# Kernel tuning notes

Hardware: AMD Instinct MI355X
Metric: run time of the kernel (lower is better)

The kernel has to match this reference:

```python
import jax, jax.numpy as jnp
import numpy as np

T, B, E, H = 2048, 2, 2048, 16
D = E // H  # 128


def setup_inputs() -> dict:
    key = jax.random.key(0)
    ks = jax.random.split(key, 4)
    query = jax.random.normal(ks[0], (T, B, E), dtype=jnp.float32)
    Wqkv = jax.random.normal(ks[1], (3 * E, E), dtype=jnp.float32) * 0.02
    bqkv = jnp.zeros((3 * E,), dtype=jnp.float32)
    Wo = jax.random.normal(ks[2], (E, E), dtype=jnp.float32) * 0.02
    bo = jnp.zeros((E,), dtype=jnp.float32)
    # Llama rotary frequencies: freqs_cis[t, j] = exp(i * t * theta^{-2j/D})
    inv_freq = 1.0 / (10000.0 ** (np.arange(0, D, 2, dtype=np.float32) / D))  # (D/2,)
    angles = np.arange(T, dtype=np.float32)[:, None] * inv_freq[None, :]       # (T, D/2)
    freqs_cos = jnp.asarray(np.cos(angles), dtype=jnp.float32)
    freqs_sin = jnp.asarray(np.sin(angles), dtype=jnp.float32)
    return {"query": query, "Wqkv": Wqkv, "bqkv": bqkv, "Wo": Wo, "bo": bo,
            "freqs_cos": freqs_cos, "freqs_sin": freqs_sin}


def _apply_rope(x, cos, sin):
    # Faithful to metaseq: x is (T, B, E) but view()-ed as (B, T, H, D);
    # jnp.reshape is the same row-major reinterpretation as torch .view().
    xr = x.reshape(B, T, H, D // 2, 2)
    x0, x1 = xr[..., 0], xr[..., 1]
    c = cos[None, :, None, :]  # broadcast over batch and heads, seq_dim=1
    s = sin[None, :, None, :]
    o0 = x0 * c - x1 * s
    o1 = x0 * s + x1 * c
    return jnp.stack([o0, o1], axis=-1).reshape(T, B, E)


def reference(query, Wqkv, bqkv, Wo, bo, freqs_cos, freqs_sin):
    # Combined QKV projection (ColumnParallelLinear, world_size=1), split order (k, v, q)
    kvq = jnp.einsum('tbe,fe->tbf', query, Wqkv) + bqkv  # (T, B, 3E)
    k, v, q = jnp.split(kvq, 3, axis=-1)
    q = _apply_rope(q, freqs_cos, freqs_sin)
    k = _apply_rope(k, freqs_cos, freqs_sin)
    # scaling split as sqrt(head_dim^-0.5) on both q and k (baddbmm path)
    s = jnp.asarray(D, jnp.float32) ** -0.25
    qb = q.reshape(T, B * H, D).swapaxes(0, 1) * s   # (BH, T, D)
    kb = k.reshape(T, B * H, D).swapaxes(0, 1) * s   # (BH, S, D)
    vb = v.reshape(T, B * H, D).swapaxes(0, 1)       # (BH, S, D)
    scores = jnp.einsum('btd,bsd->bts', qb, kb)      # (BH, T, S)
    causal = jnp.tril(jnp.ones((T, T), dtype=bool))  # ScaledUpperTriangMaskedSoftmax
    scores = jnp.where(causal[None, :, :], scores, jnp.finfo(scores.dtype).min)
    probs = jax.nn.softmax(scores, axis=-1)          # dropout p=0 -> identity
    attn = jnp.einsum('bts,bsd->btd', probs, vb)     # (BH, T, D)
    attn = attn.swapaxes(0, 1).reshape(T, B, E)
    # RowParallelLinear with skip_bias_add=True: bias returned separately (not added)
    out = jnp.einsum('tbe,fe->tbf', attn, Wo)
    return out
```

## Files before the change

### kernel.cpp

```cpp
#include <hip/hip_runtime.h>
#include <stdint.h>

typedef unsigned short u16;
typedef __attribute__((ext_vector_type(4))) float f32x4;
typedef __attribute__((ext_vector_type(8))) short bf16x8;
typedef __attribute__((ext_vector_type(8))) u16 u16x8;

#define T_SEQ  2048
#define EMB    2048
#define HD     128
#define NHEAD  16
#define NE3    6144
#define SCALE  0.29730177875068026f
#define LOG2E  1.44269504088896f

typedef __attribute__((address_space(3))) char* lds_t;
typedef const __attribute__((address_space(1))) char* gl_t;

__device__ __forceinline__ void gld16(const void* g, void* l) {
  __builtin_amdgcn_global_load_lds((gl_t)g, (lds_t)l, 16, 0, 0);
}

__device__ __forceinline__ u16 f2bf(float f) {
  union { float f; uint32_t u; } c; c.f = f;
  uint32_t r = c.u + 0x7fffu + ((c.u >> 16) & 1u);
  return (u16)(r >> 16);
}

__global__ __launch_bounds__(256) void cvt_bf16(const float* __restrict__ in,
                                                u16* __restrict__ out, int n8) {
  int i = blockIdx.x * 256 + threadIdx.x;
  if (i >= n8) return;
  const float4* p = (const float4*)in + (size_t)i * 2;
  float4 a = p[0], b = p[1];
  u16x8 o;
  o[0]=f2bf(a.x); o[1]=f2bf(a.y); o[2]=f2bf(a.z); o[3]=f2bf(a.w);
  o[4]=f2bf(b.x); o[5]=f2bf(b.y); o[6]=f2bf(b.z); o[7]=f2bf(b.w);
  *((u16x8*)out + i) = o;
}

__device__ __forceinline__ bf16x8 rdfrag(const char* slot, int row, int lq) {
  return *(const bf16x8*)(slot + row*64 + ((lq ^ ((row >> 1) & 3)) << 4));
}
__device__ __forceinline__ void stg512(const char* g, int K2, int kbyte,
                                       char* slot, int j, int tid) {
  int lb = j*8192 + tid*16;
  int row = lb >> 6, c = (lb >> 4) & 3;
  gld16(g + (size_t)row*K2 + kbyte + ((c ^ ((row >> 1) & 3)) << 4), slot + lb);
}

template<int EPI>
__global__ __launch_bounds__(512, 2) void gemmF(
    const u16* __restrict__ A, const u16* __restrict__ Bm, int K, int N,
    const float* __restrict__ cosT, const float* __restrict__ sinT,
    const float* __restrict__ bias,
    u16* __restrict__ Qh, u16* __restrict__ Kh, u16* __restrict__ Vt,
    float* __restrict__ Cout)
{
  __shared__ __align__(16) char lds[98304];
  const int tid = threadIdx.x;
  const int lane = tid & 63, w = tid >> 6;
  const int wm = w >> 2, wn = w & 3;
  const int l15 = lane & 15, lq = lane >> 4;

  const int i = blockIdx.x;
  const int r = i >> 8, x = i & 7, s = (i >> 3) & 31;
  const int regionId = r*8 + x;
  const int bM = (regionId & 3)*8 + (s >> 2);
  const int bN = (regionId >> 2)*4 + (s & 3);

  const char* Ag = (const char*)(A + (size_t)bM * 128 * K);
  const char* Bg = (const char*)(Bm + (size_t)bN * 256 * K);
  const int K2 = K * 2;
  const int nT = K >> 5;

  #define BUF(k) (lds + ((k) & 3) * 24576)
  #define STAGE(t) do { int kb_ = (t) << 6; char* b_ = BUF(t);        \
    stg512(Ag, K2, kb_, b_, 0, tid);                                  \
    stg512(Bg, K2, kb_, b_ + 8192, 0, tid);                           \
    stg512(Bg, K2, kb_, b_ + 8192, 1, tid); } while (0)

  STAGE(0); STAGE(1); STAGE(2);
  asm volatile("s_waitcnt vmcnt(6)" ::: "memory");
  __builtin_amdgcn_s_barrier();
  __builtin_amdgcn_sched_barrier(0);

  bf16x8 afA[4], bfA[4], afB[4], bfB[4];
  #pragma unroll
  for (int j = 0; j < 4; j++) afA[j] = rdfrag(BUF(0), wm*64 + j*16 + l15, lq);
  #pragma unroll
  for (int j = 0; j < 4; j++) bfA[j] = rdfrag(BUF(0) + 8192, wn*64 + j*16 + l15, lq);

  f32x4 acc[4][4] = {};

  #define ITER(t, CA, CB, OA, OB) do {                                     \
    asm volatile("s_waitcnt vmcnt(3)" ::: "memory");  \
    __builtin_amdgcn_s_barrier();                                          \
    __builtin_amdgcn_sched_barrier(0);                                     \
    const int tr_ = ((t) + 1 < nT) ? (t) + 1 : nT - 1;                     \
    const char* rb_ = BUF(tr_);                                            \
    _Pragma("unroll")                                                      \
    for (int j_ = 0; j_ < 4; j_++) OA[j_] = rdfrag(rb_, wm*64 + j_*16 + l15, lq); \
    _Pragma("unroll")                                                      \
    for (int j_ = 0; j_ < 4; j_++) OB[j_] = rdfrag(rb_ + 8192, wn*64 + j_*16 + l15, lq); \
    asm volatile("s_waitcnt lgkmcnt(8)" ::: "memory");  \
    __builtin_amdgcn_sched_barrier(0);                                     \
    const int ts_ = ((t) + 3 < nT) ? (t) + 3 : nT - 1;                     \
    STAGE(ts_);                                                            \
    __builtin_amdgcn_s_setprio(1);                                         \
    _Pragma("unroll")                                                      \
    for (int mi_ = 0; mi_ < 4; mi_++)                                      \
      _Pragma("unroll")                                                    \
      for (int ni_ = 0; ni_ < 4; ni_++)                                    \
        acc[mi_][ni_] = __builtin_amdgcn_mfma_f32_16x16x32_bf16(CA[mi_], CB[ni_], acc[mi_][ni_], 0, 0, 0); \
    __builtin_amdgcn_s_setprio(0);                                         \
  } while (0)

  for (int t = 0; t < nT; t += 2) {
    ITER(t,     afA, bfA, afB, bfB);
    ITER(t + 1, afB, bfB, afA, bfA);
  }
  asm volatile("s_waitcnt vmcnt(0) lgkmcnt(0)" ::: "memory");
  __builtin_amdgcn_sched_barrier(0);
  #undef ITER
  #undef STAGE
  #undef BUF

  if (EPI == 0) {
    #pragma unroll
    for (int mi = 0; mi < 4; mi++) {
      int row = bM*128 + wm*64 + mi*16 + lq*4;
      #pragma unroll
      for (int ni = 0; ni < 4; ni++) {
        int col = bN*256 + wn*64 + ni*16 + l15;
        #pragma unroll
        for (int rr = 0; rr < 4; rr++)
          Cout[(size_t)(row + rr) * N + col] = acc[mi][ni][rr];
      }
    }
  } else {
    const int cbase = bN*256 + wn*64;
    const int seg  = cbase >> 11;
    const int head = (cbase >> 7) & 15;
    #pragma unroll
    for (int mi = 0; mi < 4; mi++) {
      #pragma unroll
      for (int ni = 0; ni < 4; ni++) {
        int col = cbase + ni*16 + l15;
        int d = col & 127;
        float bi = bias[col];
        f32x4 v = acc[mi][ni];
        #pragma unroll
        for (int rr = 0; rr < 4; rr++) {
          int n = bM*128 + wm*64 + mi*16 + lq*4 + rr;
          float val = v[rr] + bi;
          int t = n >> 1, b = n & 1;
          int bh = b*NHEAD + head;
          if (seg == 1) {
            Vt[((size_t)bh*HD + d)*T_SEQ + t] = f2bf(val);
          } else {
            float par = __shfl_xor(val, 1);
            int fidx = d >> 1;
            float cs = cosT[(n & (T_SEQ-1))*64 + fidx];
            float sn = sinT[(n & (T_SEQ-1))*64 + fidx];
            val = (d & 1) ? (par*sn + val*cs) : (val*cs - par*sn);
            val *= SCALE;
            u16* dst = (seg == 0) ? Kh : Qh;
            dst[((size_t)bh*T_SEQ + t)*HD + d] = f2bf(val);
          }
        }
      }
    }
  }
}

#define PSW(row) ((((row) & 7) << 4) ^ (((row) & 8) << 2))

__global__ __launch_bounds__(512, 4) void attn_fwd(
    const u16* __restrict__ Qh, const u16* __restrict__ Kh,
    const u16* __restrict__ Vt, u16* __restrict__ O)
{
  const int i = blockIdx.x;
  const int kk = i >> 8, c = i & 255;
  const int b5 = c & 15;
  const int qb = kk ? (15 - b5) : b5;
  const int bh = (c >> 4) + kk * 16;

  const int tid = threadIdx.x, lane = tid & 63, w = tid >> 6;
  const int l15 = lane & 15, lq = lane >> 4;

  __shared__ u16 Ks[2][64*128];
  __shared__ u16 Vs[2][128*64];
  __shared__ char Ps[8][2048];

  const int q0 = qb*128 + w*16;
  bf16x8 qf[4];
  #pragma unroll
  for (int dc = 0; dc < 4; dc++)
    qf[dc] = *(const bf16x8*)(Qh + ((size_t)bh*T_SEQ + q0 + l15)*HD + dc*32 + lq*8);

  const int nkb = 2*qb + 2;

  #define STAGE_KV(t, b) do {                                              \
    _Pragma("unroll")                                                      \
    for (int j_ = 0; j_ < 2; j_++) {                                       \
      int lb_ = tid*16 + j_*8192;                                          \
      int row_ = lb_ >> 8, bir_ = lb_ & 255;                               \
      int sb_ = bir_ ^ ((row_ & 7) << 4);                                  \
      gld16((const char*)Kh + (((size_t)bh*T_SEQ + (t)*64 + row_) << 8) + sb_, \
            (char*)Ks[b] + lb_);                                           \
    }                                                                      \
    _Pragma("unroll")                                                      \
    for (int j_ = 0; j_ < 2; j_++) {                                       \
      int lb_ = tid*16 + j_*8192;                                          \
      int row_ = lb_ >> 7, bir_ = lb_ & 127;                               \
      int sb_ = bir_ ^ ((row_ & 7) << 4);                                  \
      gld16((const char*)Vt + ((size_t)(bh*HD + row_)*T_SEQ)*2 + (t)*128 + sb_, \
            (char*)Vs[b] + lb_);                                           \
    }                                                                      \
  } while (0)

  STAGE_KV(0, 0);
  STAGE_KV(1, 1);

  f32x4 o[8] = {};
  float m[4], l_[4];
  #pragma unroll
  for (int r = 0; r < 4; r++) { m[r] = -1e30f; l_[r] = 0.f; }

  for (int kb = 0; kb < nkb; ++kb) {
    asm volatile("s_waitcnt vmcnt(4)" ::: "memory");
    __builtin_amdgcn_s_barrier();
    __builtin_amdgcn_sched_barrier(0);

    const char* Kb = (const char*)Ks[kb & 1];
    const char* Vb = (const char*)Vs[kb & 1];

    f32x4 sacc[4];
    #pragma unroll
    for (int nf = 0; nf < 4; nf++) {
      f32x4 z = {};
      sacc[nf] = z;
      #pragma unroll
      for (int dc = 0; dc < 4; dc++) {
        int row = nf*16 + l15;
        int bir = (dc*64 + lq*16) ^ ((row & 7) << 4);
        bf16x8 kf = *(const bf16x8*)(Kb + row*256 + bir);
        sacc[nf] = __builtin_amdgcn_mfma_f32_16x16x32_bf16(qf[dc], kf, sacc[nf], 0, 0, 0);
      }
    }

    if (kb*64 + 63 > q0) {
      #pragma unroll
      for (int nf = 0; nf < 4; nf++)
        #pragma unroll
        for (int r = 0; r < 4; r++) {
          int key = kb*64 + nf*16 + l15;
          int qr  = q0 + lq*4 + r;
          if (key > qr) sacc[nf][r] = -1e30f;
        }
    }

    #pragma unroll
    for (int r = 0; r < 4; r++) {
      float mx = fmaxf(fmaxf(sacc[0][r], sacc[1][r]), fmaxf(sacc[2][r], sacc[3][r]));
      mx = fmaxf(mx, __shfl_xor(mx, 1));
      mx = fmaxf(mx, __shfl_xor(mx, 2));
      mx = fmaxf(mx, __shfl_xor(mx, 4));
      mx = fmaxf(mx, __shfl_xor(mx, 8));
      float newm = fmaxf(m[r], mx);
      float sc = exp2f((m[r] - newm) * LOG2E);
      float s = 0.f;
      #pragma unroll
      for (int nf = 0; nf < 4; nf++) {
        float p = exp2f((sacc[nf][r] - newm) * LOG2E);
        sacc[nf][r] = p;
        s += p;
      }
      l_[r] = l_[r] * sc + s;
      m[r] = newm;
      #pragma unroll
      for (int nf = 0; nf < 8; nf++) o[nf][r] *= sc;
    }

    #pragma unroll
    for (int nf = 0; nf < 4; nf++)
      #pragma unroll
      for (int r = 0; r < 4; r++) {
        int prow = lq*4 + r;
        int pbyte = prow*128 + (((nf*16 + l15)*2) ^ PSW(prow));
        *(u16*)(Ps[w] + pbyte) = f2bf(sacc[nf][r]);
      }

    #pragma unroll
    for (int kc = 0; kc < 2; kc++) {
      int pb = (kc*64 + lq*16) ^ PSW(l15);
      bf16x8 pf = *(const bf16x8*)(Ps[w] + l15*128 + pb);
      #pragma unroll
      for (int nf = 0; nf < 8; nf++) {
        int row = nf*16 + l15;
        int bir = (kc*64 + lq*16) ^ ((row & 7) << 4);
        bf16x8 vf = *(const bf16x8*)(Vb + row*128 + bir);
        o[nf] = __builtin_amdgcn_mfma_f32_16x16x32_bf16(pf, vf, o[nf], 0, 0, 0);
      }
    }

    __builtin_amdgcn_s_barrier();
    const int tnext = (kb + 2 < nkb) ? kb + 2 : nkb - 1;
    STAGE_KV(tnext, kb & 1);
  }
  asm volatile("s_waitcnt vmcnt(0)" ::: "memory");
  #undef STAGE_KV

  const int b = bh >> 4, h = bh & 15;
  #pragma unroll
  for (int r = 0; r < 4; r++) {
    float l = l_[r];
    l += __shfl_xor(l, 1);
    l += __shfl_xor(l, 2);
    l += __shfl_xor(l, 4);
    l += __shfl_xor(l, 8);
    float inv = 1.0f / l;
    int t = q0 + lq*4 + r;
    size_t base = ((size_t)(t*2 + b))*EMB + h*HD;
    #pragma unroll
    for (int nf = 0; nf < 8; nf++)
      O[base + nf*16 + l15] = f2bf(o[nf][r] * inv);
  }
}

extern "C" void kernel_launch(void* const* d_in, const int* in_sizes, int n_in,
                              void* d_out, int out_size, void* d_ws, size_t ws_size,
                              hipStream_t stream) {
  const float* query = (const float*)d_in[0];
  const float* Wqkv  = (const float*)d_in[1];
  const float* bqkv  = (const float*)d_in[2];
  const float* Wo    = (const float*)d_in[3];
  const float* fcos  = (const float*)d_in[5];
  const float* fsin  = (const float*)d_in[6];
  float* out = (float*)d_out;
  char* ws = (char*)d_ws;

  u16* WQb = (u16*)(ws + 0);
  u16* WOb = (u16*)(ws + 25165824);
  u16* A1  = (u16*)(ws + 33554432);
  u16* QH  = (u16*)(ws + 50331648);
  u16* KH  = (u16*)(ws + 67108864);
  u16* VT  = (u16*)(ws + 83886080);

  cvt_bf16<<<4096, 256, 0, stream>>>(query, A1, 1048576);
  cvt_bf16<<<6144, 256, 0, stream>>>(Wqkv, WQb, 1572864);
  cvt_bf16<<<2048, 256, 0, stream>>>(Wo,   WOb,  524288);

  gemmF<1><<<768, 512, 0, stream>>>(A1, WQb, 2048, NE3,
                                    fcos, fsin, bqkv, QH, KH, VT, nullptr);

  attn_fwd<<<512, 512, 0, stream>>>(QH, KH, VT, A1);

  gemmF<0><<<256, 512, 0, stream>>>(A1, WOb, 2048, EMB,
                                    nullptr, nullptr, nullptr,
                                    nullptr, nullptr, nullptr, out);
}
```

Measured before the change: 307.5 us.

## Use 256x256 tiles for QKV GEMM with a dedicated kernel

Splits the templated GEMM into a QKV-projection kernel and an output-projection kernel. The QKV kernel now uses 256x256 block tiles (8x4 MFMA accumulators per wave, 128 KB LDS, 4-deep buffering) and launches 384 blocks instead of 768, with a simpler single-buffered register fragment load per k-step. The goal is more arithmetic per byte loaded and less global traffic. In exchange it raises register and LDS pressure (two blocks per CU may not fit), gives fewer blocks to spread across CUs, and drops the fragment prefetch overlap.

```diff
diff --git a/kernel.cpp b/kernel.cpp
--- a/kernel.cpp
+++ b/kernel.cpp
@@ -49,12 +49,103 @@
   gld16(g + (size_t)row*K2 + kbyte + ((c ^ ((row >> 1) & 3)) << 4), slot + lb);
 }
 
-template<int EPI>
-__global__ __launch_bounds__(512, 2) void gemmF(
-    const u16* __restrict__ A, const u16* __restrict__ Bm, int K, int N,
+__global__ __launch_bounds__(512, 2) void gemmQ(
+    const u16* __restrict__ A, const u16* __restrict__ Bm, int K,
     const float* __restrict__ cosT, const float* __restrict__ sinT,
     const float* __restrict__ bias,
-    u16* __restrict__ Qh, u16* __restrict__ Kh, u16* __restrict__ Vt,
+    u16* __restrict__ Qh, u16* __restrict__ Kh, u16* __restrict__ Vt)
+{
+  __shared__ __align__(16) char lds[131072];
+  const int tid = threadIdx.x;
+  const int lane = tid & 63, w = tid >> 6;
+  const int wm = w >> 2, wn = w & 3;
+  const int l15 = lane & 15, lq = lane >> 4;
+
+  const int i = blockIdx.x;
+  const int regionId = i >> 4, s = i & 15;
+  const int bM = (regionId % 4) * 4 + (s >> 2);
+  const int bN = (regionId / 4) * 4 + (s & 3);
+
+  const char* Ag = (const char*)(A + (size_t)bM * 256 * K);
+  const char* Bg = (const char*)(Bm + (size_t)bN * 256 * K);
+  const int K2 = K * 2;
+  const int nT = K >> 5;
+
+  #define BUF(k) (lds + ((k) & 3) * 32768)
+  #define STAGE(t) do { int kb_ = (t) << 6; char* b_ = BUF(t);        \
+    stg512(Ag, K2, kb_, b_, 0, tid);                                  \
+    stg512(Ag, K2, kb_, b_, 1, tid);                                  \
+    stg512(Bg, K2, kb_, b_ + 16384, 0, tid);                          \
+    stg512(Bg, K2, kb_, b_ + 16384, 1, tid); } while (0)
+
+  STAGE(0); STAGE(1); STAGE(2);
+
+  f32x4 acc[8][4] = {};
+
+  for (int t = 0; t < nT; ++t) {
+    asm volatile("s_waitcnt vmcnt(8)" ::: "memory");
+    __builtin_amdgcn_s_barrier();
+    __builtin_amdgcn_sched_barrier(0);
+
+    const int ts = (t + 3 < nT) ? t + 3 : nT - 1;
+    STAGE(ts);
+
+    const char* rb = BUF(t);
+    bf16x8 af[8], bf[4];
+    #pragma unroll
+    for (int j = 0; j < 8; j++) af[j] = rdfrag(rb, wm*128 + j*16 + l15, lq);
+    #pragma unroll
+    for (int j = 0; j < 4; j++) bf[j] = rdfrag(rb + 16384, wn*64 + j*16 + l15, lq);
+    asm volatile("s_waitcnt lgkmcnt(0)" ::: "memory");
+    __builtin_amdgcn_sched_barrier(0);
+    __builtin_amdgcn_s_setprio(1);
+    #pragma unroll
+    for (int mi = 0; mi < 8; mi++)
+      #pragma unroll
+      for (int ni = 0; ni < 4; ni++)
+        acc[mi][ni] = __builtin_amdgcn_mfma_f32_16x16x32_bf16(af[mi], bf[ni], acc[mi][ni], 0, 0, 0);
+    __builtin_amdgcn_s_setprio(0);
+  }
+  asm volatile("s_waitcnt vmcnt(0)" ::: "memory");
+  #undef STAGE
+  #undef BUF
+
+  const int cbase = bN*256 + wn*64;
+  const int seg  = cbase >> 11;
+  const int head = (cbase >> 7) & 15;
+  #pragma unroll
+  for (int mi = 0; mi < 8; mi++) {
+    #pragma unroll
+    for (int ni = 0; ni < 4; ni++) {
+      int col = cbase + ni*16 + l15;
+      int d = col & 127;
+      float bi = bias[col];
+      f32x4 v = acc[mi][ni];
+      #pragma unroll
+      for (int rr = 0; rr < 4; rr++) {
+        int n = bM*256 + wm*128 + mi*16 + lq*4 + rr;
+        float val = v[rr] + bi;
+        int t = n >> 1, b = n & 1;
+        int bh = b*NHEAD + head;
+        if (seg == 1) {
+          Vt[((size_t)bh*HD + d)*T_SEQ + t] = f2bf(val);
+        } else {
+          float par = __shfl_xor(val, 1);
+          int fidx = d >> 1;
+          float cs = cosT[(n & (T_SEQ-1))*64 + fidx];
+          float sn = sinT[(n & (T_SEQ-1))*64 + fidx];
+          val = (d & 1) ? (par*sn + val*cs) : (val*cs - par*sn);
+          val *= SCALE;
+          u16* dst = (seg == 0) ? Kh : Qh;
+          dst[((size_t)bh*T_SEQ + t)*HD + d] = f2bf(val);
+        }
+      }
+    }
+  }
+}
+
+__global__ __launch_bounds__(512, 2) void gemmO(
+    const u16* __restrict__ A, const u16* __restrict__ Bm, int K, int N,
     float* __restrict__ Cout)
 {
   __shared__ __align__(16) char lds[98304];
@@ -94,7 +185,7 @@
   f32x4 acc[4][4] = {};
 
   #define ITER(t, CA, CB, OA, OB) do {                                     \
-    asm volatile("s_waitcnt vmcnt(3)" ::: "memory");  \
+    asm volatile("s_waitcnt vmcnt(3)" ::: "memory");                       \
     __builtin_amdgcn_s_barrier();                                          \
     __builtin_amdgcn_sched_barrier(0);                                     \
     const int tr_ = ((t) + 1 < nT) ? (t) + 1 : nT - 1;                     \
@@ -103,7 +194,7 @@
     for (int j_ = 0; j_ < 4; j_++) OA[j_] = rdfrag(rb_, wm*64 + j_*16 + l15, lq); \
     _Pragma("unroll")                                                      \
     for (int j_ = 0; j_ < 4; j_++) OB[j_] = rdfrag(rb_ + 8192, wn*64 + j_*16 + l15, lq); \
-    asm volatile("s_waitcnt lgkmcnt(8)" ::: "memory");  \
+    asm volatile("s_waitcnt lgkmcnt(8)" ::: "memory");                     \
     __builtin_amdgcn_sched_barrier(0);                                     \
     const int ts_ = ((t) + 3 < nT) ? (t) + 3 : nT - 1;                     \
     STAGE(ts_);                                                            \
@@ -126,50 +217,15 @@
   #undef STAGE
   #undef BUF
 
-  if (EPI == 0) {
-    #pragma unroll
-    for (int mi = 0; mi < 4; mi++) {
-      int row = bM*128 + wm*64 + mi*16 + lq*4;
-      #pragma unroll
-      for (int ni = 0; ni < 4; ni++) {
-        int col = bN*256 + wn*64 + ni*16 + l15;
-        #pragma unroll
-        for (int rr = 0; rr < 4; rr++)
-          Cout[(size_t)(row + rr) * N + col] = acc[mi][ni][rr];
-      }
-    }
-  } else {
-    const int cbase = bN*256 + wn*64;
-    const int seg  = cbase >> 11;
-    const int head = (cbase >> 7) & 15;
-    #pragma unroll
-    for (int mi = 0; mi < 4; mi++) {
-      #pragma unroll
-      for (int ni = 0; ni < 4; ni++) {
-        int col = cbase + ni*16 + l15;
-        int d = col & 127;
-        float bi = bias[col];
-        f32x4 v = acc[mi][ni];
-        #pragma unroll
-        for (int rr = 0; rr < 4; rr++) {
-          int n = bM*128 + wm*64 + mi*16 + lq*4 + rr;
-          float val = v[rr] + bi;
-          int t = n >> 1, b = n & 1;
-          int bh = b*NHEAD + head;
-          if (seg == 1) {
-            Vt[((size_t)bh*HD + d)*T_SEQ + t] = f2bf(val);
-          } else {
-            float par = __shfl_xor(val, 1);
-            int fidx = d >> 1;
-            float cs = cosT[(n & (T_SEQ-1))*64 + fidx];
-            float sn = sinT[(n & (T_SEQ-1))*64 + fidx];
-            val = (d & 1) ? (par*sn + val*cs) : (val*cs - par*sn);
-            val *= SCALE;
-            u16* dst = (seg == 0) ? Kh : Qh;
-            dst[((size_t)bh*T_SEQ + t)*HD + d] = f2bf(val);
-          }
-        }
-      }
+  #pragma unroll
+  for (int mi = 0; mi < 4; mi++) {
+    int row = bM*128 + wm*64 + mi*16 + lq*4;
+    #pragma unroll
+    for (int ni = 0; ni < 4; ni++) {
+      int col = bN*256 + wn*64 + ni*16 + l15;
+      #pragma unroll
+      for (int rr = 0; rr < 4; rr++)
+        Cout[(size_t)(row + rr) * N + col] = acc[mi][ni][rr];
     }
   }
 }
@@ -352,12 +408,10 @@
   cvt_bf16<<<6144, 256, 0, stream>>>(Wqkv, WQb, 1572864);
   cvt_bf16<<<2048, 256, 0, stream>>>(Wo,   WOb,  524288);
 
-  gemmF<1><<<768, 512, 0, stream>>>(A1, WQb, 2048, NE3,
-                                    fcos, fsin, bqkv, QH, KH, VT, nullptr);
+  gemmQ<<<384, 512, 0, stream>>>(A1, WQb, 2048,
+                                 fcos, fsin, bqkv, QH, KH, VT);
 
   attn_fwd<<<512, 512, 0, stream>>>(QH, KH, VT, A1);
 
-  gemmF<0><<<256, 512, 0, stream>>>(A1, WOb, 2048, EMB,
-                                    nullptr, nullptr, nullptr,
-                                    nullptr, nullptr, nullptr, out);
-}
+  gemmO<<<256, 512, 0, stream>>>(A1, WOb, 2048, EMB, out);
+}
```

After: 329.7 us. 1.07x slower.
